# Kernel tuning notes

Measured on AMD Instinct MI355X. Metric: run time of the kernel, lower is better.

Reference implementation:

```python
import jax, jax.numpy as jnp
import numpy as np

HID = 1024       # hidden_size
H = 8            # num_attention_heads
KVH = 2          # num_key_value_heads
D = HID // H     # head_dim = 128
WINDOW = 2048    # sliding_window
THETA = 10000.0  # rope_theta
B, S = 1, 4096


def rotate_half(x):
    x1, x2 = jnp.split(x, 2, axis=-1)
    return jnp.concatenate([-x2, x1], axis=-1)


def setup_inputs() -> dict:
    key = jax.random.key(0)
    ks = jax.random.split(key, 5)
    scale = 0.02
    return {
        "hidden_states": jax.random.normal(ks[0], (B, S, HID), dtype=jnp.float32),
        "wq": jax.random.normal(ks[1], (H * D, HID), dtype=jnp.float32) * scale,
        "wk": jax.random.normal(ks[2], (KVH * D, HID), dtype=jnp.float32) * scale,
        "wv": jax.random.normal(ks[3], (KVH * D, HID), dtype=jnp.float32) * scale,
        "wo": jax.random.normal(ks[4], (HID, H * D), dtype=jnp.float32) * scale,
        "position_ids": jnp.broadcast_to(jnp.arange(S, dtype=jnp.int64 if jax.config.jax_enable_x64 else jnp.int32)[None, :], (B, S)),
    }


def reference(hidden_states, wq, wk, wv, wo, position_ids):
    b, s, _ = hidden_states.shape
    # projections (torch nn.Linear: x @ W^T)
    q = (hidden_states @ wq.T).reshape(b, s, H, D).transpose(0, 2, 1, 3)      # bhsd
    k = (hidden_states @ wk.T).reshape(b, s, KVH, D).transpose(0, 2, 1, 3)    # b(kv)sd
    v = (hidden_states @ wv.T).reshape(b, s, KVH, D).transpose(0, 2, 1, 3)

    # RoPE cache (head_dim, seq_len)
    inv_freq = 1.0 / THETA ** (jnp.arange(0, D, 2, dtype=jnp.float32) / D)
    t = jnp.arange(s, dtype=jnp.float32)
    freqs = t[:, None] * inv_freq[None, :]
    emb = jnp.concatenate([freqs, freqs], axis=-1)           # (S, D)
    cos = jnp.cos(emb)[position_ids][:, None]                # (B,1,S,D)
    sin = jnp.sin(emb)[position_ids][:, None]
    q = q * cos + rotate_half(q) * sin
    k = k * cos + rotate_half(k) * sin

    # GQA: repeat kv heads to match query heads (repeat_interleave on head dim)
    groups = H // KVH
    k = jnp.repeat(k, groups, axis=1)
    v = jnp.repeat(v, groups, axis=1)

    # full score matrix with sliding-window causal mask
    scores = jnp.einsum("bhqd,bhkd->bhqk", q, k)
    i = jnp.arange(s)[:, None]
    j = jnp.arange(s)[None, :]
    mask = (j <= i) & (j > i - WINDOW)                       # causal + window
    scores = jnp.where(mask[None, None], scores, -jnp.inf) / jnp.sqrt(jnp.float32(D))

    probs = jax.nn.softmax(scores.astype(jnp.float32), axis=-1).astype(q.dtype)
    ctx = jnp.einsum("bhqk,bhkd->bhqd", probs, v)
    ctx = ctx.transpose(0, 2, 1, 3).reshape(b, s, H * D)
    return ctx @ wo.T
```

## Files before the change

kernel.cpp:

```cpp
#include <hip/hip_runtime.h>

#define S_LEN 4096
#define HIDDEN 1024
#define NH 8
#define NKV 2
#define HD 128
#define WIN 2048

typedef short bf16x8 __attribute__((ext_vector_type(8)));
typedef short bf16x4 __attribute__((ext_vector_type(4)));
typedef float f32x4 __attribute__((ext_vector_type(4)));
typedef unsigned short u16x4 __attribute__((ext_vector_type(4)));

__device__ __forceinline__ unsigned short f2b(float f) {
    unsigned int u = __builtin_bit_cast(unsigned int, f);
    u += 0x7fffu + ((u >> 16) & 1u);
    return (unsigned short)(u >> 16);
}
__device__ __forceinline__ float b2f(unsigned short u) {
    unsigned int x = ((unsigned int)u) << 16;
    return __builtin_bit_cast(float, x);
}

__device__ __forceinline__ void gl_lds16(const unsigned short* g, unsigned short* l) {
    __builtin_amdgcn_global_load_lds(
        (const __attribute__((address_space(1))) unsigned int*)g,
        (__attribute__((address_space(3))) unsigned int*)l, 16, 0, 0);
}

#define WAIT_VM6   0x0F76
#define WAIT_VM0   0x0F70
#define MEMFENCE() __asm__ volatile("" ::: "memory")

__global__ __launch_bounds__(256) void cvt5(
    const float* __restrict__ s0, unsigned short* __restrict__ t0, int n0,
    const float* __restrict__ s1, unsigned short* __restrict__ t1, int n1,
    const float* __restrict__ s2, unsigned short* __restrict__ t2, int n2,
    const float* __restrict__ s3, unsigned short* __restrict__ t3, int n3,
    const float* __restrict__ s4, unsigned short* __restrict__ t4, int n4)
{
    int i = blockIdx.x * 256 + threadIdx.x;
    const float* s; unsigned short* t;
    if (i < n0)              { s = s0; t = t0; }
    else if ((i -= n0) < n1) { s = s1; t = t1; }
    else if ((i -= n1) < n2) { s = s2; t = t2; }
    else if ((i -= n2) < n3) { s = s3; t = t3; }
    else if ((i -= n3) < n4) { s = s4; t = t4; }
    else return;
    f32x4 v = *(const f32x4*)(s + (size_t)i * 4);
    u16x4 r = { f2b(v[0]), f2b(v[1]), f2b(v[2]), f2b(v[3]) };
    *(u16x4*)(t + (size_t)i * 4) = r;
}

__global__ __launch_bounds__(256, 2) void gemm128(
    const unsigned short* __restrict__ A, const unsigned short* __restrict__ W,
    float* __restrict__ Cf, unsigned short* __restrict__ Cb,
    int M, int N, int K)
{
    __shared__ alignas(16) unsigned short As[4][64 * 32];
    __shared__ alignas(16) unsigned short Bs[4][128 * 32];

    int lane = threadIdx.x & 63;
    int w = threadIdx.x >> 6;
    int l15 = lane & 15, quad = lane >> 4;

    int tiles_n = N >> 7;
    int bid = (int)blockIdx.x;
    int nb = (int)gridDim.x;
    int lb = bid;
    if ((nb & 7) == 0) {
        int c = nb >> 3;
        lb = (bid & 7) * c + (bid >> 3);
    }
    int mt0 = lb / tiles_n;
    int nt0 = lb - mt0 * tiles_n;

    size_t goffA;
    {
        int s = w * 64 + lane;
        int row = s >> 2, spos = s & 3;
        int kblk = spos ^ ((row >> 1) & 3);
        goffA = (size_t)(mt0 * 64 + row) * K + kblk * 8;
    }
    size_t goffB[2];
    #pragma unroll
    for (int is = 0; is < 2; ++is) {
        int s = w * 128 + is * 64 + lane;
        int row = s >> 2, spos = s & 3;
        int kblk = spos ^ ((row >> 1) & 3);
        goffB[is] = (size_t)(nt0 * 128 + row) * K + kblk * 8;
    }

    int arow0 = (w >> 1) * 32;
    int brow0 = (w & 1) * 64;
    int aoff[2], boff[4];
    #pragma unroll
    for (int t = 0; t < 2; ++t) {
        int ra = arow0 + t * 16 + l15;
        aoff[t] = (ra * 4 + (quad ^ ((ra >> 1) & 3))) * 8;
    }
    #pragma unroll
    for (int j = 0; j < 4; ++j) {
        int rb = brow0 + j * 16 + l15;
        boff[j] = (rb * 4 + (quad ^ ((rb >> 1) & 3))) * 8;
    }

    f32x4 acc[2][4];
    #pragma unroll
    for (int i = 0; i < 2; ++i)
        #pragma unroll
        for (int j = 0; j < 4; ++j) acc[i][j] = (f32x4){0.f, 0.f, 0.f, 0.f};

    auto stage = [&](int i) {
        int b = i & 3, k0 = i * 32;
        gl_lds16(A + goffA + k0, &As[b][(w * 64) * 8]);
        gl_lds16(W + goffB[0] + k0, &Bs[b][(w * 128 + 0) * 8]);
        gl_lds16(W + goffB[1] + k0, &Bs[b][(w * 128 + 64) * 8]);
    };

    int nk = K >> 5;
    stage(0);
    if (nk > 1) stage(1);
    if (nk > 2) stage(2);
    for (int i = 0; i < nk; ++i) {
        MEMFENCE();
        if (i + 1 < nk) __builtin_amdgcn_s_waitcnt(WAIT_VM6);
        else            __builtin_amdgcn_s_waitcnt(WAIT_VM0);
        __builtin_amdgcn_s_barrier();
        MEMFENCE();
        if (i + 3 < nk) stage(i + 3);

        const unsigned short* Ab = &As[i & 3][0];
        const unsigned short* Bb = &Bs[i & 3][0];
        bf16x8 af[2], bf_[4];
        #pragma unroll
        for (int t = 0; t < 2; ++t) af[t]  = *(const bf16x8*)(Ab + aoff[t]);
        #pragma unroll
        for (int j = 0; j < 4; ++j) bf_[j] = *(const bf16x8*)(Bb + boff[j]);
        #pragma unroll
        for (int i2 = 0; i2 < 2; ++i2)
            #pragma unroll
            for (int j = 0; j < 4; ++j)
                acc[i2][j] = __builtin_amdgcn_mfma_f32_16x16x32_bf16(af[i2], bf_[j], acc[i2][j], 0, 0, 0);
        MEMFENCE();
    }

    #pragma unroll
    for (int i = 0; i < 2; ++i) {
        int row0 = mt0 * 64 + arow0 + i * 16 + quad * 4;
        #pragma unroll
        for (int j = 0; j < 4; ++j) {
            int col = nt0 * 128 + brow0 + j * 16 + l15;
            if (Cf) {
                #pragma unroll
                for (int reg = 0; reg < 4; ++reg)
                    Cf[(size_t)(row0 + reg) * N + col] = acc[i][j][reg];
            } else {
                #pragma unroll
                for (int reg = 0; reg < 4; ++reg)
                    Cb[(size_t)(row0 + reg) * N + col] = f2b(acc[i][j][reg]);
            }
        }
    }
}

#define QKVW (HIDDEN + 2 * NKV * HD)
__global__ __launch_bounds__(256, 3) void gemmqkv(
    const unsigned short* __restrict__ A, const unsigned short* __restrict__ W,
    const int* __restrict__ pos,
    unsigned short* __restrict__ Qb, unsigned short* __restrict__ Kb,
    unsigned short* __restrict__ Vt)
{
    __shared__ alignas(16) char pool[49152];
    unsigned short (*As)[64 * 32]  = (unsigned short (*)[64 * 32])(pool);
    unsigned short (*Bs)[128 * 32] = (unsigned short (*)[128 * 32])(pool + 16384);
    float (*Ex)[32][68] = (float (*)[32][68])(pool);
    unsigned short* T = (unsigned short*)(pool);

    int lane = threadIdx.x & 63;
    int w = threadIdx.x >> 6;
    int l15 = lane & 15, quad = lane >> 4;

    const int K = HIDDEN;
    int bid = (int)blockIdx.x;
    int lb = (bid & 7) * 96 + (bid >> 3);
    int mt0 = lb / 12;
    int nt0 = lb - mt0 * 12;

    size_t goffA;
    {
        int s = w * 64 + lane;
        int row = s >> 2, spos = s & 3;
        int kblk = spos ^ ((row >> 1) & 3);
        goffA = (size_t)(mt0 * 64 + row) * K + kblk * 8;
    }
    size_t goffB[2];
    #pragma unroll
    for (int is = 0; is < 2; ++is) {
        int s = w * 128 + is * 64 + lane;
        int row = s >> 2, spos = s & 3;
        int kblk = spos ^ ((row >> 1) & 3);
        goffB[is] = (size_t)(nt0 * 128 + row) * K + kblk * 8;
    }

    int arow0 = (w >> 1) * 32;
    int brow0 = (w & 1) * 64;
    int aoff[2], boff[4];
    #pragma unroll
    for (int t = 0; t < 2; ++t) {
        int ra = arow0 + t * 16 + l15;
        aoff[t] = (ra * 4 + (quad ^ ((ra >> 1) & 3))) * 8;
    }
    #pragma unroll
    for (int j = 0; j < 4; ++j) {
        int rb = brow0 + j * 16 + l15;
        boff[j] = (rb * 4 + (quad ^ ((rb >> 1) & 3))) * 8;
    }

    f32x4 acc[2][4];
    #pragma unroll
    for (int i = 0; i < 2; ++i)
        #pragma unroll
        for (int j = 0; j < 4; ++j) acc[i][j] = (f32x4){0.f, 0.f, 0.f, 0.f};

    auto stage = [&](int i) {
        int b = i & 3, k0 = i * 32;
        gl_lds16(A + goffA + k0, &As[b][(w * 64) * 8]);
        gl_lds16(W + goffB[0] + k0, &Bs[b][(w * 128 + 0) * 8]);
        gl_lds16(W + goffB[1] + k0, &Bs[b][(w * 128 + 64) * 8]);
    };

    stage(0);
    stage(1);
    stage(2);
    for (int i = 0; i < 32; ++i) {
        MEMFENCE();
        if (i + 1 < 32) __builtin_amdgcn_s_waitcnt(WAIT_VM6);
        else            __builtin_amdgcn_s_waitcnt(WAIT_VM0);
        __builtin_amdgcn_s_barrier();
        MEMFENCE();
        if (i + 3 < 32) stage(i + 3);

        const unsigned short* Ab = &As[i & 3][0];
        const unsigned short* Bb = &Bs[i & 3][0];
        bf16x8 af[2], bf_[4];
        #pragma unroll
        for (int t = 0; t < 2; ++t) af[t]  = *(const bf16x8*)(Ab + aoff[t]);
        #pragma unroll
        for (int j = 0; j < 4; ++j) bf_[j] = *(const bf16x8*)(Bb + boff[j]);
        #pragma unroll
        for (int i2 = 0; i2 < 2; ++i2)
            #pragma unroll
            for (int j = 0; j < 4; ++j)
                acc[i2][j] = __builtin_amdgcn_mfma_f32_16x16x32_bf16(af[i2], bf_[j], acc[i2][j], 0, 0, 0);
        MEMFENCE();
    }

    if (nt0 >= 10) {
        int kv = nt0 - 10;
        __syncthreads();
        #pragma unroll
        for (int i = 0; i < 2; ++i) {
            int srow = arow0 + i * 16 + quad * 4;
            #pragma unroll
            for (int j = 0; j < 4; ++j) {
                int d = brow0 + j * 16 + l15;
                #pragma unroll
                for (int reg = 0; reg < 4; ++reg)
                    T[(srow + reg) * 130 + d] = f2b(acc[i][j][reg]);
            }
        }
        __syncthreads();
        int tid = threadIdx.x;
        int dl = tid >> 4;
        int s4 = (tid & 15) * 4;
        #pragma unroll
        for (int it = 0; it < 8; ++it) {
            int d = it * 16 + dl;
            u16x4 v4 = { T[(s4 + 0) * 130 + d], T[(s4 + 1) * 130 + d],
                         T[(s4 + 2) * 130 + d], T[(s4 + 3) * 130 + d] };
            *(u16x4*)(Vt + (size_t)kv * HD * S_LEN + (size_t)d * S_LEN
                      + mt0 * 64 + s4) = v4;
        }
        return;
    }

    bool isQ = (nt0 < 8);
    int kv = nt0 - 8;
    bool is64 = (pos[1] == 0) && (pos[3] == 0);
    const float qscale = 0.08838834764831843f;

    float invf[4];
    #pragma unroll
    for (int j = 0; j < 4; ++j) {
        int d6 = (brow0 + j * 16 + l15) & 63;
        invf[j] = exp2f(-(float)d6 * (13.287712379549449f / 64.0f));
    }

    __syncthreads();
    #pragma unroll
    for (int i = 0; i < 2; ++i)
        #pragma unroll
        for (int j = 0; j < 4; ++j)
            #pragma unroll
            for (int reg = 0; reg < 4; ++reg)
                Ex[w][i * 16 + quad * 4 + reg][j * 16 + l15] = acc[i][j][reg];
    __syncthreads();
    #pragma unroll
    for (int i = 0; i < 2; ++i) {
        #pragma unroll
        for (int reg = 0; reg < 4; ++reg) {
            int s = mt0 * 64 + arow0 + i * 16 + quad * 4 + reg;
            int pv_ = is64 ? pos[2 * s] : pos[s];
            float pf = (float)pv_;
            #pragma unroll
            for (int j = 0; j < 4; ++j) {
                float sn, cs;
                __sincosf(pf * invf[j], &sn, &cs);
                float a  = acc[i][j][reg];
                float pr = Ex[w ^ 1][i * 16 + quad * 4 + reg][j * 16 + l15];
                int d_local = brow0 + j * 16 + l15;
                float outv = (d_local < 64) ? (a * cs - pr * sn) : (a * cs + pr * sn);
                if (isQ) {
                    Qb[(size_t)s * HIDDEN + nt0 * HD + d_local] = f2b(outv * qscale);
                } else {
                    Kb[(size_t)kv * S_LEN * HD + (size_t)s * HD + d_local] = f2b(outv);
                }
            }
        }
    }
}

__global__ __launch_bounds__(256, 2) void attn_coop(
    const unsigned short* __restrict__ Qb, const unsigned short* __restrict__ Kb,
    const unsigned short* __restrict__ Vt, unsigned short* __restrict__ Ctx)
{
    __shared__ alignas(16) unsigned short Klds[2][64 * 128];
    __shared__ alignas(16) unsigned short Vlds[2][128 * 64];

    int lane = threadIdx.x & 63;
    int w = threadIdx.x >> 6;
    int l15 = lane & 15, quad = lane >> 4;
    int h = blockIdx.y;
    int kv = h >> 2;
    int qt = (h & 4) ? (63 - (int)blockIdx.x) : (int)blockIdx.x;
    int qb = qt * 64;
    int q16 = qb + w * 16;

    bf16x8 a_q[4];
    const unsigned short* qrow = Qb + (size_t)(q16 + l15) * HIDDEN + h * HD + quad * 8;
    #pragma unroll
    for (int st = 0; st < 4; ++st) a_q[st] = *(const bf16x8*)(qrow + st * 32);

    bf16x4 ones4;
    #pragma unroll
    for (int i = 0; i < 4; ++i) ones4[i] = (short)0x3F80;

    int lo = qb - (WIN - 1); if (lo < 0) lo = 0; lo &= ~63;
    int nch = (qb + 64 - lo) >> 6;

    const unsigned short* gbase;
    unsigned short* ldsdst[2];
    int myoff[8];
    int jmul;
    if (w < 2) {
        gbase = Kb + (size_t)kv * S_LEN * HD;
        ldsdst[0] = &Klds[0][w * 8 * 512];
        ldsdst[1] = &Klds[1][w * 8 * 512];
        jmul = HD;
        #pragma unroll
        for (int tt = 0; tt < 8; ++tt) {
            int t = w * 8 + tt;
            int key  = t * 4 + (lane >> 4);
            int dblk = (lane & 15) ^ (key & 15);
            myoff[tt] = key * HD + dblk * 8;
        }
    } else {
        gbase = Vt + (size_t)kv * HD * S_LEN;
        ldsdst[0] = &Vlds[0][(w - 2) * 8 * 512];
        ldsdst[1] = &Vlds[1][(w - 2) * 8 * 512];
        jmul = 1;
        #pragma unroll
        for (int tt = 0; tt < 8; ++tt) {
            int t = (w - 2) * 8 + tt;
            int d    = t * 8 + (lane >> 3);
            int kblk = (lane & 7) ^ (d & 7);
            myoff[tt] = d * S_LEN + kblk * 8;
        }
    }

    auto issue = [&](int c) {
        int j0 = lo + c * 64;
        const unsigned short* src = gbase + (size_t)j0 * jmul;
        unsigned short* dst = ldsdst[c & 1];
        #pragma unroll
        for (int tt = 0; tt < 8; ++tt)
            gl_lds16(src + myoff[tt], dst + tt * 512);
    };

    f32x4 o[9];
    #pragma unroll
    for (int nd = 0; nd < 9; ++nd) o[nd] = (f32x4){0.f, 0.f, 0.f, 0.f};

    issue(0);

    for (int c = 0; c < nch; ++c) {
        int j0 = lo + c * 64;

        MEMFENCE();
        __builtin_amdgcn_s_waitcnt(WAIT_VM0);
        __builtin_amdgcn_s_barrier();
        MEMFENCE();
        if (c + 1 < nch) issue(c + 1);

        const unsigned short* Kc = &Klds[c & 1][0];
        const unsigned short* Vc = &Vlds[c & 1][0];

        f32x4 sc[4];
        #pragma unroll
        for (int t = 0; t < 4; ++t) {
            sc[t] = (f32x4){0.f, 0.f, 0.f, 0.f};
            int key = t * 16 + l15;
            #pragma unroll
            for (int st = 0; st < 4; ++st) {
                int off16 = key * 16 + ((st * 4 + quad) ^ (key & 15));
                bf16x8 ak = *(const bf16x8*)(Kc + off16 * 8);
                sc[t] = __builtin_amdgcn_mfma_f32_16x16x32_bf16(ak, a_q[st], sc[t], 0, 0, 0);
            }
        }

        float p[4][4];
        if (j0 + 63 <= q16 && j0 > q16 + 15 - WIN) {
            #pragma unroll
            for (int t = 0; t < 4; ++t)
                #pragma unroll
                for (int reg = 0; reg < 4; ++reg) p[t][reg] = __expf(sc[t][reg]);
        } else {
            int iq = q16 + l15;
            #pragma unroll
            for (int t = 0; t < 4; ++t) {
                #pragma unroll
                for (int reg = 0; reg < 4; ++reg) {
                    int key = j0 + t * 16 + quad * 4 + reg;
                    p[t][reg] = (key <= iq && key > iq - WIN) ? __expf(sc[t][reg]) : 0.f;
                }
            }
        }

        bf16x4 a_p[4];
        #pragma unroll
        for (int t = 0; t < 4; ++t) {
            a_p[t][0] = (short)f2b(p[t][0]);
            a_p[t][1] = (short)f2b(p[t][1]);
            a_p[t][2] = (short)f2b(p[t][2]);
            a_p[t][3] = (short)f2b(p[t][3]);
        }

        #pragma unroll
        for (int t = 0; t < 4; ++t) {
            #pragma unroll
            for (int nd = 0; nd < 8; ++nd) {
                int d = nd * 16 + l15;
                int kblk = t * 2 + (quad >> 1);
                int slot = d * 8 + (kblk ^ (d & 7));
                bf16x4 bv = *(const bf16x4*)(Vc + slot * 8 + (quad & 1) * 4);
                o[nd] = __builtin_amdgcn_mfma_f32_16x16x16bf16_1k(a_p[t], bv, o[nd], 0, 0, 0);
            }
            o[8] = __builtin_amdgcn_mfma_f32_16x16x16bf16_1k(a_p[t], ones4, o[8], 0, 0, 0);
        }
        MEMFENCE();
    }

    #pragma unroll
    for (int nd = 0; nd < 8; ++nd) {
        int d = nd * 16 + l15;
        #pragma unroll
        for (int reg = 0; reg < 4; ++reg) {
            int q = q16 + quad * 4 + reg;
            Ctx[(size_t)q * HIDDEN + h * HD + d] = f2b(o[nd][reg] / o[8][reg]);
        }
    }
}

extern "C" void kernel_launch(void* const* d_in, const int* in_sizes, int n_in,
                              void* d_out, int out_size, void* d_ws, size_t ws_size,
                              hipStream_t stream)
{
    const float* hidden = (const float*)d_in[0];
    const float* wq = (const float*)d_in[1];
    const float* wk = (const float*)d_in[2];
    const float* wv = (const float*)d_in[3];
    const float* wo = (const float*)d_in[4];
    const int* pos = (const int*)d_in[5];
    float* out = (float*)d_out;

    char* ws = (char*)d_ws;
    size_t off = 0;
    unsigned short* Hb   = (unsigned short*)(ws + off); off += (size_t)S_LEN * HIDDEN * 2;
    unsigned short* Wqkv = (unsigned short*)(ws + off); off += (size_t)QKVW * HIDDEN * 2;
    unsigned short* Wob  = (unsigned short*)(ws + off); off += (size_t)HIDDEN * HIDDEN * 2;
    unsigned short* Qb   = (unsigned short*)(ws + off); off += (size_t)S_LEN * HIDDEN * 2;
    unsigned short* Kb   = (unsigned short*)(ws + off); off += (size_t)S_LEN * NKV * HD * 2;
    unsigned short* Vt   = (unsigned short*)(ws + off); off += (size_t)S_LEN * NKV * HD * 2;
    unsigned short* Cb   = (unsigned short*)(ws + off); off += (size_t)S_LEN * HIDDEN * 2;

    const int n_h  = S_LEN * HIDDEN / 4;
    const int n_wq = HIDDEN * HIDDEN / 4;
    const int n_wk = NKV * HD * HIDDEN / 4;
    int tot4 = n_h + n_wq + 2 * n_wk + n_wq;
    cvt5<<<(tot4 + 255) / 256, 256, 0, stream>>>(
        hidden, Hb, n_h,
        wq, Wqkv, n_wq,
        wk, Wqkv + (size_t)HIDDEN * HIDDEN, n_wk,
        wv, Wqkv + (size_t)(HIDDEN + NKV * HD) * HIDDEN, n_wk,
        wo, Wob, n_wq);

    gemmqkv<<<(S_LEN / 64) * 12, 256, 0, stream>>>(
        Hb, Wqkv, pos, Qb, Kb, Vt);

    attn_coop<<<dim3(S_LEN / 64, NH), 256, 0, stream>>>(Qb, Kb, Vt, Cb);

    gemm128<<<(S_LEN / 64) * (HIDDEN / 128), 256, 0, stream>>>(
        Cb, Wob, out, nullptr, S_LEN, HIDDEN, HIDDEN);
}
```

Measured before the change: 183.7 us.

## Deepen GEMM LDS pipeline to six buffers with two k-steps per barrier

Both GEMM kernels (output projection and fused QKV) move from a 4-deep LDS ring with one 32-wide k-step per barrier to a 6-deep ring that processes two k-steps per barrier and issues two stages per iteration. This halves the barrier count and keeps more loads in flight. It also raises wave priority around the MFMA bursts with s_setprio. The cost is more shared memory: gemmqkv grows to 72KB and its launch bound drops from 3 to 2 blocks per CU, which lowers occupancy. The waitcnt values were not updated for the two-stage issue pattern, so the wait depth may be off and cause a hazard or stall. The loop also assumes nk is even.

```diff
diff --git a/kernel.cpp b/kernel.cpp
--- a/kernel.cpp
+++ b/kernel.cpp
@@ -57,8 +57,8 @@
     float* __restrict__ Cf, unsigned short* __restrict__ Cb,
     int M, int N, int K)
 {
-    __shared__ alignas(16) unsigned short As[4][64 * 32];
-    __shared__ alignas(16) unsigned short Bs[4][128 * 32];
+    __shared__ alignas(16) unsigned short As[6][64 * 32];
+    __shared__ alignas(16) unsigned short Bs[6][128 * 32];
 
     int lane = threadIdx.x & 63;
     int w = threadIdx.x >> 6;
@@ -111,37 +111,49 @@
         #pragma unroll
         for (int j = 0; j < 4; ++j) acc[i][j] = (f32x4){0.f, 0.f, 0.f, 0.f};
 
-    auto stage = [&](int i) {
-        int b = i & 3, k0 = i * 32;
+    auto stage = [&](int s, int b) {
+        int k0 = s * 32;
         gl_lds16(A + goffA + k0, &As[b][(w * 64) * 8]);
         gl_lds16(W + goffB[0] + k0, &Bs[b][(w * 128 + 0) * 8]);
         gl_lds16(W + goffB[1] + k0, &Bs[b][(w * 128 + 64) * 8]);
     };
 
     int nk = K >> 5;
-    stage(0);
-    if (nk > 1) stage(1);
-    if (nk > 2) stage(2);
-    for (int i = 0; i < nk; ++i) {
-        MEMFENCE();
-        if (i + 1 < nk) __builtin_amdgcn_s_waitcnt(WAIT_VM6);
+    int np = nk >> 1;
+    if (nk > 0) stage(0, 0);
+    if (nk > 1) stage(1, 1);
+    if (nk > 2) stage(2, 2);
+    if (nk > 3) stage(3, 3);
+    int cb = 0, sb = 4;
+    for (int j = 0; j < np; ++j) {
+        MEMFENCE();
+        if (j + 1 < np) __builtin_amdgcn_s_waitcnt(WAIT_VM6);
         else            __builtin_amdgcn_s_waitcnt(WAIT_VM0);
         __builtin_amdgcn_s_barrier();
         MEMFENCE();
-        if (i + 3 < nk) stage(i + 3);
-
-        const unsigned short* Ab = &As[i & 3][0];
-        const unsigned short* Bb = &Bs[i & 3][0];
-        bf16x8 af[2], bf_[4];
-        #pragma unroll
-        for (int t = 0; t < 2; ++t) af[t]  = *(const bf16x8*)(Ab + aoff[t]);
-        #pragma unroll
-        for (int j = 0; j < 4; ++j) bf_[j] = *(const bf16x8*)(Bb + boff[j]);
-        #pragma unroll
-        for (int i2 = 0; i2 < 2; ++i2)
-            #pragma unroll
-            for (int j = 0; j < 4; ++j)
-                acc[i2][j] = __builtin_amdgcn_mfma_f32_16x16x32_bf16(af[i2], bf_[j], acc[i2][j], 0, 0, 0);
+        int s0 = 2 * j + 4;
+        if (s0 < nk)     stage(s0, sb);
+        if (s0 + 1 < nk) stage(s0 + 1, sb + 1 == 6 ? 0 : sb + 1);
+        sb += 2; if (sb >= 6) sb -= 6;
+
+        #pragma unroll
+        for (int half = 0; half < 2; ++half) {
+            const unsigned short* Ab = &As[cb + half][0];
+            const unsigned short* Bb = &Bs[cb + half][0];
+            bf16x8 af[2], bf_[4];
+            #pragma unroll
+            for (int t = 0; t < 2; ++t) af[t]  = *(const bf16x8*)(Ab + aoff[t]);
+            #pragma unroll
+            for (int jj = 0; jj < 4; ++jj) bf_[jj] = *(const bf16x8*)(Bb + boff[jj]);
+            __builtin_amdgcn_s_setprio(1);
+            #pragma unroll
+            for (int i2 = 0; i2 < 2; ++i2)
+                #pragma unroll
+                for (int jj = 0; jj < 4; ++jj)
+                    acc[i2][jj] = __builtin_amdgcn_mfma_f32_16x16x32_bf16(af[i2], bf_[jj], acc[i2][jj], 0, 0, 0);
+            __builtin_amdgcn_s_setprio(0);
+        }
+        cb += 2; if (cb >= 6) cb -= 6;
         MEMFENCE();
     }
 
@@ -165,15 +177,15 @@
 }
 
 #define QKVW (HIDDEN + 2 * NKV * HD)
-__global__ __launch_bounds__(256, 3) void gemmqkv(
+__global__ __launch_bounds__(256, 2) void gemmqkv(
     const unsigned short* __restrict__ A, const unsigned short* __restrict__ W,
     const int* __restrict__ pos,
     unsigned short* __restrict__ Qb, unsigned short* __restrict__ Kb,
     unsigned short* __restrict__ Vt)
 {
-    __shared__ alignas(16) char pool[49152];
+    __shared__ alignas(16) char pool[73728];
     unsigned short (*As)[64 * 32]  = (unsigned short (*)[64 * 32])(pool);
-    unsigned short (*Bs)[128 * 32] = (unsigned short (*)[128 * 32])(pool + 16384);
+    unsigned short (*Bs)[128 * 32] = (unsigned short (*)[128 * 32])(pool + 24576);
     float (*Ex)[32][68] = (float (*)[32][68])(pool);
     unsigned short* T = (unsigned short*)(pool);
 
@@ -223,36 +235,47 @@
         #pragma unroll
         for (int j = 0; j < 4; ++j) acc[i][j] = (f32x4){0.f, 0.f, 0.f, 0.f};
 
-    auto stage = [&](int i) {
-        int b = i & 3, k0 = i * 32;
+    auto stage = [&](int s, int b) {
+        int k0 = s * 32;
         gl_lds16(A + goffA + k0, &As[b][(w * 64) * 8]);
         gl_lds16(W + goffB[0] + k0, &Bs[b][(w * 128 + 0) * 8]);
         gl_lds16(W + goffB[1] + k0, &Bs[b][(w * 128 + 64) * 8]);
     };
 
-    stage(0);
-    stage(1);
-    stage(2);
-    for (int i = 0; i < 32; ++i) {
-        MEMFENCE();
-        if (i + 1 < 32) __builtin_amdgcn_s_waitcnt(WAIT_VM6);
-        else            __builtin_amdgcn_s_waitcnt(WAIT_VM0);
+    stage(0, 0);
+    stage(1, 1);
+    stage(2, 2);
+    stage(3, 3);
+    int cb = 0, sb = 4;
+    for (int j = 0; j < 16; ++j) {
+        MEMFENCE();
+        if (j < 15) __builtin_amdgcn_s_waitcnt(WAIT_VM6);
+        else        __builtin_amdgcn_s_waitcnt(WAIT_VM0);
         __builtin_amdgcn_s_barrier();
         MEMFENCE();
-        if (i + 3 < 32) stage(i + 3);
-
-        const unsigned short* Ab = &As[i & 3][0];
-        const unsigned short* Bb = &Bs[i & 3][0];
-        bf16x8 af[2], bf_[4];
-        #pragma unroll
-        for (int t = 0; t < 2; ++t) af[t]  = *(const bf16x8*)(Ab + aoff[t]);
-        #pragma unroll
-        for (int j = 0; j < 4; ++j) bf_[j] = *(const bf16x8*)(Bb + boff[j]);
-        #pragma unroll
-        for (int i2 = 0; i2 < 2; ++i2)
-            #pragma unroll
-            for (int j = 0; j < 4; ++j)
-                acc[i2][j] = __builtin_amdgcn_mfma_f32_16x16x32_bf16(af[i2], bf_[j], acc[i2][j], 0, 0, 0);
+        int s0 = 2 * j + 4;
+        if (s0 < 32)     stage(s0, sb);
+        if (s0 + 1 < 32) stage(s0 + 1, sb + 1 == 6 ? 0 : sb + 1);
+        sb += 2; if (sb >= 6) sb -= 6;
+
+        #pragma unroll
+        for (int half = 0; half < 2; ++half) {
+            const unsigned short* Ab = &As[cb + half][0];
+            const unsigned short* Bb = &Bs[cb + half][0];
+            bf16x8 af[2], bf_[4];
+            #pragma unroll
+            for (int t = 0; t < 2; ++t) af[t]  = *(const bf16x8*)(Ab + aoff[t]);
+            #pragma unroll
+            for (int jj = 0; jj < 4; ++jj) bf_[jj] = *(const bf16x8*)(Bb + boff[jj]);
+            __builtin_amdgcn_s_setprio(1);
+            #pragma unroll
+            for (int i2 = 0; i2 < 2; ++i2)
+                #pragma unroll
+                for (int jj = 0; jj < 4; ++jj)
+                    acc[i2][jj] = __builtin_amdgcn_mfma_f32_16x16x32_bf16(af[i2], bf_[jj], acc[i2][jj], 0, 0, 0);
+            __builtin_amdgcn_s_setprio(0);
+        }
+        cb += 2; if (cb >= 6) cb -= 6;
         MEMFENCE();
     }
 
```

Result: no change. 180.2 us (median of 2 runs) (-1.9%).

## Enlarge GEMM tiles to 128x128 and raise MFMA wave priority

Applied to the files above, without the earlier changes.

Both the QKV projection GEMM and the output GEMM move from 64x128 to 128x128 block tiles. Each wave now computes a 64x64 sub-tile with a 4x4 accumulator grid, and the staging, waitcnt thresholds, epilogue and RoPE/V-transpose indexing are adjusted to match. s_setprio is placed around the MFMA block. The larger tile doubles operand reuse per LDS load and halves the grid. In exchange it raises register and LDS use (occupancy drops to 2 blocks per CU) and launches fewer blocks (384 and 256) on a large-CU device, which risks under-filling the GPU.

```diff
diff --git a/kernel.cpp b/kernel.cpp
--- a/kernel.cpp
+++ b/kernel.cpp
@@ -28,7 +28,8 @@
         (__attribute__((address_space(3))) unsigned int*)l, 16, 0, 0);
 }
 
-#define WAIT_VM6   0x0F76
+#define WAIT_VM8   0x0F78
+#define WAIT_VM4   0x0F74
 #define WAIT_VM0   0x0F70
 #define MEMFENCE() __asm__ volatile("" ::: "memory")
 
@@ -57,7 +58,7 @@
     float* __restrict__ Cf, unsigned short* __restrict__ Cb,
     int M, int N, int K)
 {
-    __shared__ alignas(16) unsigned short As[4][64 * 32];
+    __shared__ alignas(16) unsigned short As[4][128 * 32];
     __shared__ alignas(16) unsigned short Bs[4][128 * 32];
 
     int lane = threadIdx.x & 63;
@@ -75,47 +76,39 @@
     int mt0 = lb / tiles_n;
     int nt0 = lb - mt0 * tiles_n;
 
-    size_t goffA;
-    {
-        int s = w * 64 + lane;
+    size_t goffA[2], goffB[2];
+    #pragma unroll
+    for (int is = 0; is < 2; ++is) {
+        int s = is * 256 + w * 64 + lane;
         int row = s >> 2, spos = s & 3;
         int kblk = spos ^ ((row >> 1) & 3);
-        goffA = (size_t)(mt0 * 64 + row) * K + kblk * 8;
-    }
-    size_t goffB[2];
-    #pragma unroll
-    for (int is = 0; is < 2; ++is) {
-        int s = w * 128 + is * 64 + lane;
-        int row = s >> 2, spos = s & 3;
-        int kblk = spos ^ ((row >> 1) & 3);
+        goffA[is] = (size_t)(mt0 * 128 + row) * K + kblk * 8;
         goffB[is] = (size_t)(nt0 * 128 + row) * K + kblk * 8;
     }
 
-    int arow0 = (w >> 1) * 32;
+    int arow0 = (w >> 1) * 64;
     int brow0 = (w & 1) * 64;
-    int aoff[2], boff[4];
-    #pragma unroll
-    for (int t = 0; t < 2; ++t) {
+    int aoff[4], boff[4];
+    #pragma unroll
+    for (int t = 0; t < 4; ++t) {
         int ra = arow0 + t * 16 + l15;
         aoff[t] = (ra * 4 + (quad ^ ((ra >> 1) & 3))) * 8;
-    }
-    #pragma unroll
-    for (int j = 0; j < 4; ++j) {
-        int rb = brow0 + j * 16 + l15;
-        boff[j] = (rb * 4 + (quad ^ ((rb >> 1) & 3))) * 8;
-    }
-
-    f32x4 acc[2][4];
-    #pragma unroll
-    for (int i = 0; i < 2; ++i)
+        int rb = brow0 + t * 16 + l15;
+        boff[t] = (rb * 4 + (quad ^ ((rb >> 1) & 3))) * 8;
+    }
+
+    f32x4 acc[4][4];
+    #pragma unroll
+    for (int i = 0; i < 4; ++i)
         #pragma unroll
         for (int j = 0; j < 4; ++j) acc[i][j] = (f32x4){0.f, 0.f, 0.f, 0.f};
 
-    auto stage = [&](int i) {
-        int b = i & 3, k0 = i * 32;
-        gl_lds16(A + goffA + k0, &As[b][(w * 64) * 8]);
-        gl_lds16(W + goffB[0] + k0, &Bs[b][(w * 128 + 0) * 8]);
-        gl_lds16(W + goffB[1] + k0, &Bs[b][(w * 128 + 64) * 8]);
+    auto stage = [&](int s) {
+        int b = s & 3, k0 = s * 32;
+        gl_lds16(A + goffA[0] + k0, &As[b][(w * 64) * 8]);
+        gl_lds16(A + goffA[1] + k0, &As[b][(256 + w * 64) * 8]);
+        gl_lds16(W + goffB[0] + k0, &Bs[b][(w * 64) * 8]);
+        gl_lds16(W + goffB[1] + k0, &Bs[b][(256 + w * 64) * 8]);
     };
 
     int nk = K >> 5;
@@ -124,30 +117,33 @@
     if (nk > 2) stage(2);
     for (int i = 0; i < nk; ++i) {
         MEMFENCE();
-        if (i + 1 < nk) __builtin_amdgcn_s_waitcnt(WAIT_VM6);
-        else            __builtin_amdgcn_s_waitcnt(WAIT_VM0);
+        if (i + 2 < nk)      __builtin_amdgcn_s_waitcnt(WAIT_VM8);
+        else if (i + 1 < nk) __builtin_amdgcn_s_waitcnt(WAIT_VM4);
+        else                 __builtin_amdgcn_s_waitcnt(WAIT_VM0);
         __builtin_amdgcn_s_barrier();
         MEMFENCE();
         if (i + 3 < nk) stage(i + 3);
 
         const unsigned short* Ab = &As[i & 3][0];
         const unsigned short* Bb = &Bs[i & 3][0];
-        bf16x8 af[2], bf_[4];
-        #pragma unroll
-        for (int t = 0; t < 2; ++t) af[t]  = *(const bf16x8*)(Ab + aoff[t]);
+        bf16x8 af[4], bf_[4];
+        #pragma unroll
+        for (int t = 0; t < 4; ++t) af[t]  = *(const bf16x8*)(Ab + aoff[t]);
         #pragma unroll
         for (int j = 0; j < 4; ++j) bf_[j] = *(const bf16x8*)(Bb + boff[j]);
-        #pragma unroll
-        for (int i2 = 0; i2 < 2; ++i2)
+        __builtin_amdgcn_s_setprio(1);
+        #pragma unroll
+        for (int i2 = 0; i2 < 4; ++i2)
             #pragma unroll
             for (int j = 0; j < 4; ++j)
                 acc[i2][j] = __builtin_amdgcn_mfma_f32_16x16x32_bf16(af[i2], bf_[j], acc[i2][j], 0, 0, 0);
-        MEMFENCE();
-    }
-
-    #pragma unroll
-    for (int i = 0; i < 2; ++i) {
-        int row0 = mt0 * 64 + arow0 + i * 16 + quad * 4;
+        __builtin_amdgcn_s_setprio(0);
+        MEMFENCE();
+    }
+
+    #pragma unroll
+    for (int i = 0; i < 4; ++i) {
+        int row0 = mt0 * 128 + arow0 + i * 16 + quad * 4;
         #pragma unroll
         for (int j = 0; j < 4; ++j) {
             int col = nt0 * 128 + brow0 + j * 16 + l15;
@@ -165,16 +161,16 @@
 }
 
 #define QKVW (HIDDEN + 2 * NKV * HD)
-__global__ __launch_bounds__(256, 3) void gemmqkv(
+__global__ __launch_bounds__(256, 2) void gemmqkv(
     const unsigned short* __restrict__ A, const unsigned short* __restrict__ W,
     const int* __restrict__ pos,
     unsigned short* __restrict__ Qb, unsigned short* __restrict__ Kb,
     unsigned short* __restrict__ Vt)
 {
-    __shared__ alignas(16) char pool[49152];
-    unsigned short (*As)[64 * 32]  = (unsigned short (*)[64 * 32])(pool);
-    unsigned short (*Bs)[128 * 32] = (unsigned short (*)[128 * 32])(pool + 16384);
-    float (*Ex)[32][68] = (float (*)[32][68])(pool);
+    __shared__ alignas(16) char pool[65536];
+    unsigned short (*As)[128 * 32] = (unsigned short (*)[128 * 32])(pool);
+    unsigned short (*Bs)[128 * 32] = (unsigned short (*)[128 * 32])(pool + 32768);
+    float (*Ex)[64][64] = (float (*)[64][64])(pool);
     unsigned short* T = (unsigned short*)(pool);
 
     int lane = threadIdx.x & 63;
@@ -183,51 +179,43 @@
 
     const int K = HIDDEN;
     int bid = (int)blockIdx.x;
-    int lb = (bid & 7) * 96 + (bid >> 3);
+    int lb = (bid & 7) * 48 + (bid >> 3);
     int mt0 = lb / 12;
     int nt0 = lb - mt0 * 12;
 
-    size_t goffA;
-    {
-        int s = w * 64 + lane;
+    size_t goffA[2], goffB[2];
+    #pragma unroll
+    for (int is = 0; is < 2; ++is) {
+        int s = is * 256 + w * 64 + lane;
         int row = s >> 2, spos = s & 3;
         int kblk = spos ^ ((row >> 1) & 3);
-        goffA = (size_t)(mt0 * 64 + row) * K + kblk * 8;
-    }
-    size_t goffB[2];
-    #pragma unroll
-    for (int is = 0; is < 2; ++is) {
-        int s = w * 128 + is * 64 + lane;
-        int row = s >> 2, spos = s & 3;
-        int kblk = spos ^ ((row >> 1) & 3);
+        goffA[is] = (size_t)(mt0 * 128 + row) * K + kblk * 8;
         goffB[is] = (size_t)(nt0 * 128 + row) * K + kblk * 8;
     }
 
-    int arow0 = (w >> 1) * 32;
+    int arow0 = (w >> 1) * 64;
     int brow0 = (w & 1) * 64;
-    int aoff[2], boff[4];
-    #pragma unroll
-    for (int t = 0; t < 2; ++t) {
+    int aoff[4], boff[4];
+    #pragma unroll
+    for (int t = 0; t < 4; ++t) {
         int ra = arow0 + t * 16 + l15;
         aoff[t] = (ra * 4 + (quad ^ ((ra >> 1) & 3))) * 8;
-    }
-    #pragma unroll
-    for (int j = 0; j < 4; ++j) {
-        int rb = brow0 + j * 16 + l15;
-        boff[j] = (rb * 4 + (quad ^ ((rb >> 1) & 3))) * 8;
-    }
-
-    f32x4 acc[2][4];
-    #pragma unroll
-    for (int i = 0; i < 2; ++i)
+        int rb = brow0 + t * 16 + l15;
+        boff[t] = (rb * 4 + (quad ^ ((rb >> 1) & 3))) * 8;
+    }
+
+    f32x4 acc[4][4];
+    #pragma unroll
+    for (int i = 0; i < 4; ++i)
         #pragma unroll
         for (int j = 0; j < 4; ++j) acc[i][j] = (f32x4){0.f, 0.f, 0.f, 0.f};
 
-    auto stage = [&](int i) {
-        int b = i & 3, k0 = i * 32;
-        gl_lds16(A + goffA + k0, &As[b][(w * 64) * 8]);
-        gl_lds16(W + goffB[0] + k0, &Bs[b][(w * 128 + 0) * 8]);
-        gl_lds16(W + goffB[1] + k0, &Bs[b][(w * 128 + 64) * 8]);
+    auto stage = [&](int s) {
+        int b = s & 3, k0 = s * 32;
+        gl_lds16(A + goffA[0] + k0, &As[b][(w * 64) * 8]);
+        gl_lds16(A + goffA[1] + k0, &As[b][(256 + w * 64) * 8]);
+        gl_lds16(W + goffB[0] + k0, &Bs[b][(w * 64) * 8]);
+        gl_lds16(W + goffB[1] + k0, &Bs[b][(256 + w * 64) * 8]);
     };
 
     stage(0);
@@ -235,24 +223,27 @@
     stage(2);
     for (int i = 0; i < 32; ++i) {
         MEMFENCE();
-        if (i + 1 < 32) __builtin_amdgcn_s_waitcnt(WAIT_VM6);
-        else            __builtin_amdgcn_s_waitcnt(WAIT_VM0);
+        if (i + 2 < 32)      __builtin_amdgcn_s_waitcnt(WAIT_VM8);
+        else if (i + 1 < 32) __builtin_amdgcn_s_waitcnt(WAIT_VM4);
+        else                 __builtin_amdgcn_s_waitcnt(WAIT_VM0);
         __builtin_amdgcn_s_barrier();
         MEMFENCE();
         if (i + 3 < 32) stage(i + 3);
 
         const unsigned short* Ab = &As[i & 3][0];
         const unsigned short* Bb = &Bs[i & 3][0];
-        bf16x8 af[2], bf_[4];
-        #pragma unroll
-        for (int t = 0; t < 2; ++t) af[t]  = *(const bf16x8*)(Ab + aoff[t]);
+        bf16x8 af[4], bf_[4];
+        #pragma unroll
+        for (int t = 0; t < 4; ++t) af[t]  = *(const bf16x8*)(Ab + aoff[t]);
         #pragma unroll
         for (int j = 0; j < 4; ++j) bf_[j] = *(const bf16x8*)(Bb + boff[j]);
-        #pragma unroll
-        for (int i2 = 0; i2 < 2; ++i2)
+        __builtin_amdgcn_s_setprio(1);
+        #pragma unroll
+        for (int i2 = 0; i2 < 4; ++i2)
             #pragma unroll
             for (int j = 0; j < 4; ++j)
                 acc[i2][j] = __builtin_amdgcn_mfma_f32_16x16x32_bf16(af[i2], bf_[j], acc[i2][j], 0, 0, 0);
+        __builtin_amdgcn_s_setprio(0);
         MEMFENCE();
     }
 
@@ -260,7 +251,7 @@
         int kv = nt0 - 10;
         __syncthreads();
         #pragma unroll
-        for (int i = 0; i < 2; ++i) {
+        for (int i = 0; i < 4; ++i) {
             int srow = arow0 + i * 16 + quad * 4;
             #pragma unroll
             for (int j = 0; j < 4; ++j) {
@@ -272,15 +263,15 @@
         }
         __syncthreads();
         int tid = threadIdx.x;
-        int dl = tid >> 4;
-        int s4 = (tid & 15) * 4;
-        #pragma unroll
-        for (int it = 0; it < 8; ++it) {
-            int d = it * 16 + dl;
+        int dl = tid >> 5;
+        int s4 = (tid & 31) * 4;
+        #pragma unroll
+        for (int it = 0; it < 16; ++it) {
+            int d = it * 8 + dl;
             u16x4 v4 = { T[(s4 + 0) * 130 + d], T[(s4 + 1) * 130 + d],
                          T[(s4 + 2) * 130 + d], T[(s4 + 3) * 130 + d] };
             *(u16x4*)(Vt + (size_t)kv * HD * S_LEN + (size_t)d * S_LEN
-                      + mt0 * 64 + s4) = v4;
+                      + mt0 * 128 + s4) = v4;
         }
         return;
     }
@@ -299,7 +290,7 @@
 
     __syncthreads();
     #pragma unroll
-    for (int i = 0; i < 2; ++i)
+    for (int i = 0; i < 4; ++i)
         #pragma unroll
         for (int j = 0; j < 4; ++j)
             #pragma unroll
@@ -307,10 +298,10 @@
                 Ex[w][i * 16 + quad * 4 + reg][j * 16 + l15] = acc[i][j][reg];
     __syncthreads();
     #pragma unroll
-    for (int i = 0; i < 2; ++i) {
+    for (int i = 0; i < 4; ++i) {
         #pragma unroll
         for (int reg = 0; reg < 4; ++reg) {
-            int s = mt0 * 64 + arow0 + i * 16 + quad * 4 + reg;
+            int s = mt0 * 128 + arow0 + i * 16 + quad * 4 + reg;
             int pv_ = is64 ? pos[2 * s] : pos[s];
             float pf = (float)pv_;
             #pragma unroll
@@ -515,11 +506,11 @@
         wv, Wqkv + (size_t)(HIDDEN + NKV * HD) * HIDDEN, n_wk,
         wo, Wob, n_wq);
 
-    gemmqkv<<<(S_LEN / 64) * 12, 256, 0, stream>>>(
+    gemmqkv<<<(S_LEN / 128) * 12, 256, 0, stream>>>(
         Hb, Wqkv, pos, Qb, Kb, Vt);
 
     attn_coop<<<dim3(S_LEN / 64, NH), 256, 0, stream>>>(Qb, Kb, Vt, Cb);
 
-    gemm128<<<(S_LEN / 64) * (HIDDEN / 128), 256, 0, stream>>>(
+    gemm128<<<(S_LEN / 128) * (HIDDEN / 128), 256, 0, stream>>>(
         Cb, Wob, out, nullptr, S_LEN, HIDDEN, HIDDEN);
 }
```

After: 184.3 us. About the same (+0.3%).
